# Kernel optimization log

Measured on AMD Instinct MI355X. Metric: run time of the kernel, lower is better.

The kernel has to match this reference:

```python
import jax, jax.numpy as jnp
import numpy as np


def _hat(w):
    # w [...,3] -> skew-symmetric [...,3,3]
    x, y, z = w[..., 0], w[..., 1], w[..., 2]
    o = jnp.zeros_like(x)
    return jnp.stack([
        jnp.stack([o, -z, y], -1),
        jnp.stack([z, o, -x], -1),
        jnp.stack([-y, x, o], -1)], -2)


def _expmap(twist):
    # SE(3) exponential map. twist [...,6] = (v, w); returns [...,4,4]
    v, w = twist[..., :3], twist[..., 3:]
    th = jnp.linalg.norm(w, axis=-1, keepdims=True)[..., None]  # [...,1,1]
    Wh = _hat(w)
    W2 = Wh @ Wh
    small = th < 1e-4
    safe = jnp.where(small, 1.0, th)
    A = jnp.where(small, 1.0 - th * th / 6.0, jnp.sin(safe) / safe)
    Bc = jnp.where(small, 0.5 - th * th / 24.0, (1.0 - jnp.cos(safe)) / (safe * safe))
    Cc = jnp.where(small, 1.0 / 6.0 - th * th / 120.0, (safe - jnp.sin(safe)) / (safe ** 3))
    I = jnp.eye(3, dtype=twist.dtype)
    R = I + A * Wh + Bc * W2
    V = I + Bc * Wh + Cc * W2
    t = (V @ v[..., None])[..., 0]
    top = jnp.concatenate([R, t[..., None]], -1)  # [...,3,4]
    bot = jnp.broadcast_to(jnp.array([0.0, 0.0, 0.0, 1.0], twist.dtype), top.shape[:-2] + (1, 4))
    return jnp.concatenate([top, bot], -2)


def setup_inputs() -> dict:
    key = jax.random.key(0)
    ks = jax.random.split(key, 5)
    B, C, H, W = 2, 16, 32, 32
    embeddings = 0.3 * jax.random.normal(ks[0], (B, C, H, W), jnp.float32)
    revisions = 0.1 * jax.random.normal(ks[1], (B, 3, H, W), jnp.float32)
    weights = jax.random.uniform(ks[2], (B, 3, H, W), jnp.float32, 0.1, 1.0)
    depth = jax.random.uniform(ks[3], (B, 1, H, W), jnp.float32, 1.0, 5.0)
    pix = (jnp.zeros((4, 4), jnp.float32)
           .at[0, 0].set(float(W)).at[1, 1].set(float(W))
           .at[0, 2].set(W / 2.0).at[1, 2].set(H / 2.0)
           .at[2, 2].set(1.0).at[3, 3].set(1.0))
    pix_T_camXs = jnp.tile(pix[None], (B, 1, 1))
    twists = 0.02 * jax.random.normal(ks[4], (B, H, W, 6), jnp.float32)
    Tmat = _expmap(twists)  # valid SE(3) per pixel [B,H,W,4,4]
    return dict(embeddings=embeddings, revisions=revisions, weights=weights,
                depth=depth, pix_T_camXs=pix_T_camXs, Tmat=Tmat)


def reference(embeddings, revisions, weights, depth, pix_T_camXs, Tmat):
    B, C, H, W = embeddings.shape
    N = H * W
    dt = embeddings.dtype

    # pairwise embedding affinity exp(-||e_i - e_k||_2)  [B,N,N]
    e = embeddings.reshape(B, C, N).transpose(0, 2, 1)  # [B,N,C]
    diff = e[:, :, None, :] - e[:, None, :, :]
    aff = jnp.exp(-jnp.linalg.norm(diff, axis=-1))

    fx, fy = pix_T_camXs[:, 0, 0], pix_T_camXs[:, 1, 1]
    x0, y0 = pix_T_camXs[:, 0, 2], pix_T_camXs[:, 1, 2]

    # depth -> pointcloud [B,N,3]
    ys, xs = jnp.meshgrid(jnp.arange(H, dtype=dt), jnp.arange(W, dtype=dt), indexing='ij')
    u, v = xs.reshape(-1), ys.reshape(-1)
    z = depth.reshape(B, N)
    X = (u[None] - x0[:, None]) * z / fx[:, None]
    Y = (v[None] - y0[:, None]) * z / fy[:, None]
    xyz = jnp.stack([X, Y, z], -1)

    T = Tmat.reshape(B, N, 4, 4)
    Rm, tv = T[..., :3, :3], T[..., :3, 3]
    # T_k applied to its own point, and T_i (anchor) applied to every point
    TjXj = jnp.einsum('bkpq,bkq->bkp', Rm, xyz) + tv                    # [B,N,3]
    TiXj = jnp.einsum('bipq,bkq->bikp', Rm, xyz) + tv[:, :, None, :]     # [B,Ni,Nk,3]

    def pie(P):
        # projection (u, v, 1/Z)
        sh = (B,) + (1,) * (P.ndim - 2)
        invz = 1.0 / P[..., 2]
        uu = fx.reshape(sh) * P[..., 0] * invz + x0.reshape(sh)
        vv = fy.reshape(sh) * P[..., 1] * invz + y0.reshape(sh)
        return jnp.stack([uu, vv, invz], -1)

    pie_TjXj = pie(TjXj)   # [B,N,3]
    pie_TiXj = pie(TiXj)   # [B,Ni,Nk,3]

    r = revisions.reshape(B, 3, N).transpose(0, 2, 1)                   # [B,N,3]
    residual = pie_TiXj - (pie_TjXj + r)[:, None]                       # [B,Ni,Nk,3]

    # projection Jacobian wrt 3D point, d = 1/Z of transformed point
    d = pie_TiXj[..., 2]
    Xp, Yp = TiXj[..., 0], TiXj[..., 1]
    sh = (B, 1, 1)
    fxr, fyr = fx.reshape(sh), fy.reshape(sh)
    z0 = jnp.zeros_like(d)
    Jp = jnp.stack([
        jnp.stack([fxr * d, z0, -fxr * Xp * d * d], -1),
        jnp.stack([z0, fyr * d, -fyr * Yp * d * d], -1),
        jnp.stack([z0, z0, -d * d], -1)], -2)                            # [B,Ni,Nk,3,3]

    # transformation Jacobian [I | hat(X)]  [B,Nk,3,6]
    I3 = jnp.broadcast_to(jnp.eye(3, dtype=dt), (B, N, 3, 3))
    JT = jnp.concatenate([I3, _hat(xyz)], -1)

    Jac = jnp.einsum('bikpq,bkqr->bikpr', Jp, JT)                        # [B,Ni,Nk,3,6]

    wflat = weights.reshape(B, 3, N).transpose(0, 2, 1)                  # [B,Nk,3]
    wts = aff[..., None] * wflat[:, None]                                # [B,Ni,Nk,3]

    WJ = wts[..., None] * Jac
    Hm = jnp.einsum('bikcp,bikcq->bipq', WJ, Jac)                        # [B,Ni,6,6]
    rhs = jnp.einsum('bikcp,bikc->bip', Jac, residual)                   # [B,Ni,6]

    delta = jnp.einsum('bipq,biq->bip', jnp.linalg.inv(Hm), rhs)         # [B,N,6]

    dT = _expmap(delta.reshape(B, H, W, 6))                              # [B,H,W,4,4]
    return dT @ Tmat
```

## Files before the change

kernel.cpp:

```cpp
#include <hip/hip_runtime.h>
#include <math.h>

#define BB 2
#define CC 16
#define HH 32
#define WW 32
#define NN (HH*WW)
#define NPX (BB*NN)
#define PH  512

__global__ __launch_bounds__(256, 2)
void dse3_mono(const float* __restrict__ emb,
               const float* __restrict__ rev,
               const float* __restrict__ wgt,
               const float* __restrict__ dep,
               const float* __restrict__ pix,
               const float* __restrict__ Tm,
               float* __restrict__ out)
{
    __shared__ float4 sE0[PH], sE1[PH], sE2[PH], sE3[PH], sQ0[PH], sQ1[PH];
    __shared__ float2 sQ2[PH];

    int tid  = threadIdx.x;
    int lane = tid & 63;
    int wv   = tid >> 6;
    int px   = blockIdx.x * 4 + wv;
    int b    = px >> 10;
    int kpx  = px & (NN - 1);

    float fx = pix[b*16 + 0], fy = pix[b*16 + 5];
    float x0 = pix[b*16 + 2], y0 = pix[b*16 + 6];
    float ifx = __builtin_amdgcn_rcpf(fx);
    float ify = __builtin_amdgcn_rcpf(fy);

    float ei[16];
    float sei = 0.f;
    #pragma unroll
    for (int c = 0; c < 16; ++c) {
        ei[c] = emb[(size_t)b*CC*NN + (size_t)c*NN + kpx];
        sei += ei[c]*ei[c];
    }
    const float4* Tp4 = (const float4*)(Tm + (size_t)px * 16);
    float4 Tr0 = Tp4[0], Tr1 = Tp4[1], Tr2 = Tp4[2];

    float aM0=0.f, aM2=0.f, aM4=0.f, aM5=0.f, aM8=0.f;
    float aN0=0.f, aN1=0.f, aN2=0.f, aN3=0.f, aN4=0.f,
          aN5=0.f, aN6=0.f, aN7=0.f, aN8=0.f;
    float aP0=0.f, aP1=0.f, aP2=0.f, aP3=0.f, aP4=0.f, aP5=0.f;
    float aR0=0.f, aR1=0.f, aR2=0.f, aR3=0.f, aR4=0.f, aR5=0.f;

    #pragma unroll
    for (int phase = 0; phase < 2; ++phase) {
        #pragma unroll
        for (int rr = 0; rr < 2; ++rr) {
            int r  = rr*256 + tid;
            int k  = phase*PH + r;
            int gk = b*NN + k;

            float se = 0.f;
            float ev[16];
            #pragma unroll
            for (int c = 0; c < 16; ++c) {
                ev[c] = emb[(size_t)b*CC*NN + (size_t)c*NN + k];
                se += ev[c]*ev[c];
            }
            float u = (float)(k & (WW - 1));
            float v = (float)((k & (NN-1)) >> 5);
            float z = dep[b*NN + k];
            float X = (u - x0) * z * ifx;
            float Y = (v - y0) * z * ify;

            const float4* T4 = (const float4*)(Tm + (size_t)gk * 16);
            float4 t0 = T4[0], t1 = T4[1], t2 = T4[2];
            float Tx = t0.x*X + t0.y*Y + t0.z*z + t0.w;
            float Ty = t1.x*X + t1.y*Y + t1.z*z + t1.w;
            float Tz = t2.x*X + t2.y*Y + t2.z*z + t2.w;
            float di = __builtin_amdgcn_rcpf(Tz);

            float p0 = fx*Tx*di + x0 + rev[(size_t)b*3*NN + 0*NN + k];
            float p1 = fy*Ty*di + y0 + rev[(size_t)b*3*NN + 1*NN + k];
            float p2 = di            + rev[(size_t)b*3*NN + 2*NN + k];
            float w0 = wgt[(size_t)b*3*NN + 0*NN + k];
            float w1 = wgt[(size_t)b*3*NN + 1*NN + k];
            float w2 = wgt[(size_t)b*3*NN + 2*NN + k];

            sE0[r] = make_float4(ev[0],  ev[1],  ev[2],  ev[3]);
            sE1[r] = make_float4(ev[4],  ev[5],  ev[6],  ev[7]);
            sE2[r] = make_float4(ev[8],  ev[9],  ev[10], ev[11]);
            sE3[r] = make_float4(ev[12], ev[13], ev[14], ev[15]);
            sQ0[r] = make_float4(X, Y, z, p0);
            sQ1[r] = make_float4(p1, p2, w0, w1);
            sQ2[r] = make_float2(w2, se);
        }
        __syncthreads();

        #pragma unroll 2
        for (int j = 0; j < 8; ++j) {
            int r = j*64 + lane;

            float4 k0 = sE0[r], k1 = sE1[r], k2 = sE2[r], k3 = sE3[r];
            float4 q0 = sQ0[r], q1 = sQ1[r];
            float2 q2 = sQ2[r];

            float d0 = k0.x*ei[0]  + k0.y*ei[1]  + k0.z*ei[2]  + k0.w*ei[3];
            float d1 = k1.x*ei[4]  + k1.y*ei[5]  + k1.z*ei[6]  + k1.w*ei[7];
            float d2 = k2.x*ei[8]  + k2.y*ei[9]  + k2.z*ei[10] + k2.w*ei[11];
            float d3 = k3.x*ei[12] + k3.y*ei[13] + k3.z*ei[14] + k3.w*ei[15];
            float dot = (d0 + d1) + (d2 + d3);
            float ssq = fmaxf(sei + q2.y - 2.f*dot, 0.f);
            float aff = __expf(-__builtin_amdgcn_sqrtf(ssq));

            float X = q0.x, Y = q0.y, Z = q0.z;
            float Tx = Tr0.x*X + Tr0.y*Y + Tr0.z*Z + Tr0.w;
            float Ty = Tr1.x*X + Tr1.y*Y + Tr1.z*Z + Tr1.w;
            float Tz = Tr2.x*X + Tr2.y*Y + Tr2.z*Z + Tr2.w;
            float di = __builtin_amdgcn_rcpf(Tz);

            float a =  fx*di;
            float e =  fy*di;
            float uu = a*Tx;
            float vv = e*Ty;
            float r0 = uu + x0 - q0.w;
            float r1 = vv + y0 - q1.x;
            float r2 = di      - q1.y;
            float c = -uu*di;
            float f = -vv*di;
            float g = -di*di;

            float y0v = a*r0;
            float y1v = e*r1;
            float y2v = c*r0 + f*r1 + g*r2;
            aR0 += y0v; aR1 += y1v; aR2 += y2v;
            aR3 += Z*y1v - Y*y2v;
            aR4 += X*y2v - Z*y0v;
            aR5 += Y*y0v - X*y1v;

            float w0 = aff*q1.z, w1 = aff*q1.w, w2 = aff*q2.x;
            float aw = w0*a, ew = w1*e;
            float m00 = aw*a, m02 = aw*c;
            float m11 = ew*e, m12 = ew*f;
            float m22 = w0*c*c + w1*f*f + w2*g*g;
            aM0 += m00; aM2 += m02; aM4 += m11; aM5 += m12; aM8 += m22;

            float n00 = -m02*Y;
            float n01 =  m02*X - m00*Z;
            float n02 =  m00*Y;
            float n10 =  m11*Z - m12*Y;
            float n11 =  m12*X;
            float n12 = -m11*X;
            float n20 =  m12*Z - m22*Y;
            float n21 =  m22*X - m02*Z;
            float n22 =  m02*Y - m12*X;
            aN0 += n00; aN1 += n01; aN2 += n02;
            aN3 += n10; aN4 += n11; aN5 += n12;
            aN6 += n20; aN7 += n21; aN8 += n22;

            aP0 += Z*n10 - Y*n20;
            aP1 += Z*n11 - Y*n21;
            aP2 += Z*n12 - Y*n22;
            aP3 += X*n21 - Z*n01;
            aP4 += X*n22 - Z*n02;
            aP5 += Y*n02 - X*n12;
        }
        __syncthreads();
    }

    float acc[26] = { aM0,aM2,aM4,aM5,aM8,
                      aN0,aN1,aN2,aN3,aN4,aN5,aN6,aN7,aN8,
                      aP0,aP1,aP2,aP3,aP4,aP5,
                      aR0,aR1,aR2,aR3,aR4,aR5 };
    #pragma unroll
    for (int off = 32; off > 0; off >>= 1)
        #pragma unroll
        for (int t = 0; t < 26; ++t)
            acc[t] += __shfl_xor(acc[t], off, 64);

    if (lane != 0) return;

    float am[6][6];
    am[0][0]=acc[0]; am[0][1]=0.f;    am[0][2]=acc[1];
    am[1][1]=acc[2]; am[1][2]=acc[3]; am[2][2]=acc[4];
    am[0][3]=acc[5];  am[0][4]=acc[6];  am[0][5]=acc[7];
    am[1][3]=acc[8];  am[1][4]=acc[9];  am[1][5]=acc[10];
    am[2][3]=acc[11]; am[2][4]=acc[12]; am[2][5]=acc[13];
    am[3][3]=acc[14]; am[3][4]=acc[15]; am[3][5]=acc[16];
    am[4][4]=acc[17]; am[4][5]=acc[18]; am[5][5]=acc[19];
    #pragma unroll
    for (int p = 0; p < 6; ++p)
        #pragma unroll
        for (int q = 0; q < p; ++q) am[p][q] = am[q][p];
    float rh[6] = { acc[20], acc[21], acc[22], acc[23], acc[24], acc[25] };

    float L[6][6], dinv[6];
    #pragma unroll
    for (int p = 0; p < 6; ++p) {
        #pragma unroll
        for (int q = 0; q <= p; ++q) {
            float sm = am[p][q];
            #pragma unroll
            for (int r = 0; r < q; ++r) sm -= L[p][r]*L[q][r];
            if (q == p) {
                float sq = __builtin_amdgcn_sqrtf(sm);
                L[p][p] = sq;
                dinv[p] = __builtin_amdgcn_rcpf(sq);
            } else {
                L[p][q] = sm * dinv[q];
            }
        }
    }
    float yv[6];
    #pragma unroll
    for (int p = 0; p < 6; ++p) {
        float sm = rh[p];
        #pragma unroll
        for (int r = 0; r < p; ++r) sm -= L[p][r]*yv[r];
        yv[p] = sm * dinv[p];
    }
    float sol[6];
    #pragma unroll
    for (int pi = 5; pi >= 0; --pi) {
        float sm = yv[pi];
        #pragma unroll
        for (int r = pi + 1; r < 6; ++r) sm -= L[r][pi]*sol[r];
        sol[pi] = sm * dinv[pi];
    }

    float vx = sol[0], vy = sol[1], vz = sol[2];
    float wx = sol[3], wy = sol[4], wz = sol[5];
    float th2 = wx*wx + wy*wy + wz*wz;
    float th  = __builtin_amdgcn_sqrtf(th2);
    float Ae, Be, Ce;
    if (th < 1e-4f) {
        Ae = 1.0f - th2*(1.0f/6.0f);
        Be = 0.5f - th2*(1.0f/24.0f);
        Ce = 1.0f/6.0f - th2*(1.0f/120.0f);
    } else {
        float sn = __sinf(th), cn = __cosf(th);
        float ith = __builtin_amdgcn_rcpf(th), ith2 = ith*ith;
        Ae = sn*ith;
        Be = (1.0f - cn)*ith2;
        Ce = (th - sn)*ith2*ith;
    }
    float Wh[3][3] = {{0.f,-wz, wy},{ wz,0.f,-wx},{-wy, wx,0.f}};
    float W2[3][3] = {{wx*wx - th2, wx*wy,       wx*wz      },
                      {wx*wy,       wy*wy - th2, wy*wz      },
                      {wx*wz,       wy*wz,       wz*wz - th2}};
    float Rd[3][3], Vd[3][3];
    #pragma unroll
    for (int p = 0; p < 3; ++p)
        #pragma unroll
        for (int q = 0; q < 3; ++q) {
            float idq = (p == q) ? 1.0f : 0.0f;
            Rd[p][q] = idq + Ae*Wh[p][q] + Be*W2[p][q];
            Vd[p][q] = idq + Be*Wh[p][q] + Ce*W2[p][q];
        }
    float td[3];
    #pragma unroll
    for (int p = 0; p < 3; ++p)
        td[p] = Vd[p][0]*vx + Vd[p][1]*vy + Vd[p][2]*vz;

    const float4 bot = Tp4[3];
    float* o = out + (size_t)px * 16;
    #pragma unroll
    for (int p = 0; p < 3; ++p) {
        float4 r;
        float4 Ta = (p==0)?Tr0:((p==1)?Tr1:Tr2);  (void)Ta;
        r.x = Rd[p][0]*Tr0.x + Rd[p][1]*Tr1.x + Rd[p][2]*Tr2.x + td[p]*bot.x;
        r.y = Rd[p][0]*Tr0.y + Rd[p][1]*Tr1.y + Rd[p][2]*Tr2.y + td[p]*bot.y;
        r.z = Rd[p][0]*Tr0.z + Rd[p][1]*Tr1.z + Rd[p][2]*Tr2.z + td[p]*bot.z;
        r.w = Rd[p][0]*Tr0.w + Rd[p][1]*Tr1.w + Rd[p][2]*Tr2.w + td[p]*bot.w;
        *(float4*)(o + p*4) = r;
    }
    *(float4*)(o + 12) = bot;
}

extern "C" void kernel_launch(void* const* d_in, const int* in_sizes, int n_in,
                              void* d_out, int out_size, void* d_ws, size_t ws_size,
                              hipStream_t stream) {
    const float* emb = (const float*)d_in[0];
    const float* rev = (const float*)d_in[1];
    const float* wgt = (const float*)d_in[2];
    const float* dep = (const float*)d_in[3];
    const float* pix = (const float*)d_in[4];
    const float* Tm  = (const float*)d_in[5];
    float* out = (float*)d_out;

    dse3_mono<<<NPX/4, 256, 0, stream>>>(emb, rev, wgt, dep, pix, Tm, out);
}
```

Baseline: 23.75 us.

## Split each pixel's reduction across two waves and pack embeddings as fp16 dot2

Each output pixel's sum over all source pixels is now split between two waves, which combine their partial sums through LDS. The grid doubles and launch bounds request four blocks per CU. Embeddings are stored in LDS as packed fp16 pairs, and the affinity dot product uses the fdot2 instruction, which halves the LDS footprint and the embedding read traffic. In exchange, every block redoes the full staging of source-pixel data for only two output pixels instead of four. The fp16 rounding also changes the affinity values slightly.

```diff
diff --git a/kernel.cpp b/kernel.cpp
--- a/kernel.cpp
+++ b/kernel.cpp
@@ -9,22 +9,38 @@
 #define NPX (BB*NN)
 #define PH  512
 
-__global__ __launch_bounds__(256, 2)
-void dse3_mono(const float* __restrict__ emb,
-               const float* __restrict__ rev,
-               const float* __restrict__ wgt,
-               const float* __restrict__ dep,
-               const float* __restrict__ pix,
-               const float* __restrict__ Tm,
-               float* __restrict__ out)
+typedef _Float16 half2_t __attribute__((ext_vector_type(2)));
+
+__device__ __forceinline__ float h2f_dot(float packed_a, half2_t b, float c) {
+    half2_t a = __builtin_bit_cast(half2_t, packed_a);
+#if __has_builtin(__builtin_amdgcn_fdot2)
+    return __builtin_amdgcn_fdot2(a, b, c, false);
+#else
+    return c + (float)a.x*(float)b.x + (float)a.y*(float)b.y;
+#endif
+}
+
+__global__ __launch_bounds__(256, 4)
+void dse3_mono2(const float* __restrict__ emb,
+                const float* __restrict__ rev,
+                const float* __restrict__ wgt,
+                const float* __restrict__ dep,
+                const float* __restrict__ pix,
+                const float* __restrict__ Tm,
+                float* __restrict__ out)
 {
-    __shared__ float4 sE0[PH], sE1[PH], sE2[PH], sE3[PH], sQ0[PH], sQ1[PH];
+    __shared__ float4 sE4[PH*2];
+    __shared__ float4 sQ0[PH];
+    __shared__ float4 sQ1[PH];
     __shared__ float2 sQ2[PH];
+    __shared__ float  ldsR[4][26];
 
     int tid  = threadIdx.x;
     int lane = tid & 63;
     int wv   = tid >> 6;
-    int px   = blockIdx.x * 4 + wv;
+    int s    = wv >> 1;
+    int h    = wv & 1;
+    int px   = blockIdx.x * 2 + s;
     int b    = px >> 10;
     int kpx  = px & (NN - 1);
 
@@ -33,12 +49,16 @@
     float ifx = __builtin_amdgcn_rcpf(fx);
     float ify = __builtin_amdgcn_rcpf(fy);
 
-    float ei[16];
+    half2_t eih[8];
     float sei = 0.f;
     #pragma unroll
-    for (int c = 0; c < 16; ++c) {
-        ei[c] = emb[(size_t)b*CC*NN + (size_t)c*NN + kpx];
-        sei += ei[c]*ei[c];
+    for (int c = 0; c < 8; ++c) {
+        float f0 = emb[(size_t)b*CC*NN + (size_t)(2*c  )*NN + kpx];
+        float f1 = emb[(size_t)b*CC*NN + (size_t)(2*c+1)*NN + kpx];
+        half2_t hp; hp.x = (_Float16)f0; hp.y = (_Float16)f1;
+        eih[c] = hp;
+        float r0 = (float)hp.x, r1 = (float)hp.y;
+        sei += r0*r0 + r1*r1;
     }
     const float4* Tp4 = (const float4*)(Tm + (size_t)px * 16);
     float4 Tr0 = Tp4[0], Tr1 = Tp4[1], Tr2 = Tp4[2];
@@ -58,11 +78,15 @@
             int gk = b*NN + k;
 
             float se = 0.f;
-            float ev[16];
+            float pk[8];
             #pragma unroll
-            for (int c = 0; c < 16; ++c) {
-                ev[c] = emb[(size_t)b*CC*NN + (size_t)c*NN + k];
-                se += ev[c]*ev[c];
+            for (int c = 0; c < 8; ++c) {
+                float f0 = emb[(size_t)b*CC*NN + (size_t)(2*c  )*NN + k];
+                float f1 = emb[(size_t)b*CC*NN + (size_t)(2*c+1)*NN + k];
+                half2_t hp; hp.x = (_Float16)f0; hp.y = (_Float16)f1;
+                pk[c] = __builtin_bit_cast(float, hp);
+                float r0 = (float)hp.x, r1 = (float)hp.y;
+                se += r0*r0 + r1*r1;
             }
             float u = (float)(k & (WW - 1));
             float v = (float)((k & (NN-1)) >> 5);
@@ -84,29 +108,31 @@
             float w1 = wgt[(size_t)b*3*NN + 1*NN + k];
             float w2 = wgt[(size_t)b*3*NN + 2*NN + k];
 
-            sE0[r] = make_float4(ev[0],  ev[1],  ev[2],  ev[3]);
-            sE1[r] = make_float4(ev[4],  ev[5],  ev[6],  ev[7]);
-            sE2[r] = make_float4(ev[8],  ev[9],  ev[10], ev[11]);
-            sE3[r] = make_float4(ev[12], ev[13], ev[14], ev[15]);
+            sE4[r*2 + 0] = make_float4(pk[0], pk[1], pk[2], pk[3]);
+            sE4[r*2 + 1] = make_float4(pk[4], pk[5], pk[6], pk[7]);
             sQ0[r] = make_float4(X, Y, z, p0);
             sQ1[r] = make_float4(p1, p2, w0, w1);
             sQ2[r] = make_float2(w2, se);
         }
         __syncthreads();
 
-        #pragma unroll 2
-        for (int j = 0; j < 8; ++j) {
-            int r = j*64 + lane;
-
-            float4 k0 = sE0[r], k1 = sE1[r], k2 = sE2[r], k3 = sE3[r];
+        #pragma unroll
+        for (int j = 0; j < 4; ++j) {
+            int r = h*256 + j*64 + lane;
+
+            float4 ea = sE4[r*2 + 0], eb = sE4[r*2 + 1];
             float4 q0 = sQ0[r], q1 = sQ1[r];
             float2 q2 = sQ2[r];
 
-            float d0 = k0.x*ei[0]  + k0.y*ei[1]  + k0.z*ei[2]  + k0.w*ei[3];
-            float d1 = k1.x*ei[4]  + k1.y*ei[5]  + k1.z*ei[6]  + k1.w*ei[7];
-            float d2 = k2.x*ei[8]  + k2.y*ei[9]  + k2.z*ei[10] + k2.w*ei[11];
-            float d3 = k3.x*ei[12] + k3.y*ei[13] + k3.z*ei[14] + k3.w*ei[15];
-            float dot = (d0 + d1) + (d2 + d3);
+            float dot = 0.f;
+            dot = h2f_dot(ea.x, eih[0], dot);
+            dot = h2f_dot(ea.y, eih[1], dot);
+            dot = h2f_dot(ea.z, eih[2], dot);
+            dot = h2f_dot(ea.w, eih[3], dot);
+            dot = h2f_dot(eb.x, eih[4], dot);
+            dot = h2f_dot(eb.y, eih[5], dot);
+            dot = h2f_dot(eb.z, eih[6], dot);
+            dot = h2f_dot(eb.w, eih[7], dot);
             float ssq = fmaxf(sei + q2.y - 2.f*dot, 0.f);
             float aff = __expf(-__builtin_amdgcn_sqrtf(ssq));
 
@@ -175,21 +201,31 @@
         for (int t = 0; t < 26; ++t)
             acc[t] += __shfl_xor(acc[t], off, 64);
 
-    if (lane != 0) return;
+    if (lane == 0)
+        #pragma unroll
+        for (int t = 0; t < 26; ++t) ldsR[wv][t] = acc[t];
+    __syncthreads();
+
+    if ((tid & 127) != 0) return;
+    int ss = tid >> 7;
+
+    float hv[26];
+    #pragma unroll
+    for (int t = 0; t < 26; ++t) hv[t] = ldsR[2*ss][t] + ldsR[2*ss+1][t];
 
     float am[6][6];
-    am[0][0]=acc[0]; am[0][1]=0.f;    am[0][2]=acc[1];
-    am[1][1]=acc[2]; am[1][2]=acc[3]; am[2][2]=acc[4];
-    am[0][3]=acc[5];  am[0][4]=acc[6];  am[0][5]=acc[7];
-    am[1][3]=acc[8];  am[1][4]=acc[9];  am[1][5]=acc[10];
-    am[2][3]=acc[11]; am[2][4]=acc[12]; am[2][5]=acc[13];
-    am[3][3]=acc[14]; am[3][4]=acc[15]; am[3][5]=acc[16];
-    am[4][4]=acc[17]; am[4][5]=acc[18]; am[5][5]=acc[19];
+    am[0][0]=hv[0]; am[0][1]=0.f;    am[0][2]=hv[1];
+    am[1][1]=hv[2]; am[1][2]=hv[3];  am[2][2]=hv[4];
+    am[0][3]=hv[5];  am[0][4]=hv[6];  am[0][5]=hv[7];
+    am[1][3]=hv[8];  am[1][4]=hv[9];  am[1][5]=hv[10];
+    am[2][3]=hv[11]; am[2][4]=hv[12]; am[2][5]=hv[13];
+    am[3][3]=hv[14]; am[3][4]=hv[15]; am[3][5]=hv[16];
+    am[4][4]=hv[17]; am[4][5]=hv[18]; am[5][5]=hv[19];
     #pragma unroll
     for (int p = 0; p < 6; ++p)
         #pragma unroll
         for (int q = 0; q < p; ++q) am[p][q] = am[q][p];
-    float rh[6] = { acc[20], acc[21], acc[22], acc[23], acc[24], acc[25] };
+    float rh[6] = { hv[20], hv[21], hv[22], hv[23], hv[24], hv[25] };
 
     float L[6][6], dinv[6];
     #pragma unroll
@@ -264,7 +300,6 @@
     #pragma unroll
     for (int p = 0; p < 3; ++p) {
         float4 r;
-        float4 Ta = (p==0)?Tr0:((p==1)?Tr1:Tr2);  (void)Ta;
         r.x = Rd[p][0]*Tr0.x + Rd[p][1]*Tr1.x + Rd[p][2]*Tr2.x + td[p]*bot.x;
         r.y = Rd[p][0]*Tr0.y + Rd[p][1]*Tr1.y + Rd[p][2]*Tr2.y + td[p]*bot.y;
         r.z = Rd[p][0]*Tr0.z + Rd[p][1]*Tr1.z + Rd[p][2]*Tr2.z + td[p]*bot.z;
@@ -285,5 +320,5 @@
     const float* Tm  = (const float*)d_in[5];
     float* out = (float*)d_out;
 
-    dse3_mono<<<NPX/4, 256, 0, stream>>>(emb, rev, wgt, dep, pix, Tm, out);
+    dse3_mono2<<<NPX/2, 256, 0, stream>>>(emb, rev, wgt, dep, pix, Tm, out);
 }
```

After: 68.38 us. +187.9%, slower.
